# Kernel optimization log

Hardware: AMD Instinct MI355X
Metric: run time of the kernel (lower is better)

Reference implementation:

```python
import jax, jax.numpy as jnp
import numpy as np

N_NODES = 50000
E_HALF = 500000
N_FEAT = 5
GCN_DIMS = [32, 64, 128]
MLP_DIMS = [128, 64]


def _lin_init(key, fan_in, fan_out):
    return jax.random.normal(key, (fan_in, fan_out), dtype=jnp.float32) / np.sqrt(fan_in)


def setup_inputs() -> dict:
    key = jax.random.key(0)
    ks = jax.random.split(key, 20)
    x = jax.random.normal(ks[0], (N_NODES, N_FEAT), dtype=jnp.float32)
    src = jax.random.randint(ks[1], (E_HALF,), 0, N_NODES)
    dst = jax.random.randint(ks[2], (E_HALF,), 0, N_NODES)
    # paired edges: second half is the reversed direction of the first half
    edges = jnp.stack([jnp.concatenate([src, dst]), jnp.concatenate([dst, src])], axis=0).astype(jnp.int64)
    edge_attr = jax.random.uniform(ks[3], (2 * E_HALF, 2), dtype=jnp.float32)
    detector_labels = jnp.ones((N_NODES,), dtype=bool)
    inp = {"x": x, "edges": edges, "edge_attr": edge_attr, "detector_labels": detector_labels}
    # GraphConv params: out = agg @ w_rel + x @ w_root + b
    dims = [N_FEAT] + GCN_DIMS
    for i, (di, do) in enumerate(zip(dims[:-1], dims[1:])):
        inp[f"w_rel{i}"] = _lin_init(ks[4 + 3 * i], di, do)
        inp[f"w_root{i}"] = _lin_init(ks[5 + 3 * i], di, do)
        inp[f"b{i}"] = jnp.zeros((do,), dtype=jnp.float32)
    # edge MLP: transition_dim = 2*128 + 1 = 257
    mdims = [2 * GCN_DIMS[-1] + 1] + MLP_DIMS
    for i, (di, do) in enumerate(zip(mdims[:-1], mdims[1:])):
        inp[f"w_d{i}"] = _lin_init(ks[13 + 2 * i], di, do)
        inp[f"b_d{i}"] = jnp.zeros((do,), dtype=jnp.float32)
    inp["w_out"] = _lin_init(ks[17], MLP_DIMS[-1], 1)
    inp["b_out"] = jnp.zeros((1,), dtype=jnp.float32)
    return inp


def reference(x, edges, edge_attr, detector_labels,
              w_rel0, w_root0, b0, w_rel1, w_root1, b1, w_rel2, w_root2, b2,
              w_d0, b_d0, w_d1, b_d1, w_out, b_out):
    n = x.shape[0]
    src, dst = edges[0], edges[1]
    w = edge_attr[:, 0] * edge_attr[:, 1]  # [E]

    def gconv(h, wr, wro, b):
        msg = h[src] * w[:, None]                                   # gather + scale  [E, d]
        agg = jax.ops.segment_sum(msg, dst, num_segments=n)          # scatter-add     [N, d]
        return jnp.tanh(agg @ wr + h @ wro + b)

    h = gconv(x, w_rel0, w_root0, b0)
    h = gconv(h, w_rel1, w_root1, b1)
    h = gconv(h, w_rel2, w_root2, b2)

    # SplitSyndromes: keep edges whose both endpoints are detector nodes
    # (indices are concrete, so this is computed with numpy -> static shapes)
    e_np = np.asarray(edges)
    subset = np.arange(n)[np.asarray(detector_labels)]
    valid = np.isin(e_np, subset).sum(axis=0) == 2
    keep = np.nonzero(valid)[0]
    edges_f = jnp.asarray(e_np[:, keep])
    ea = edge_attr[keep]

    ef = jnp.concatenate([h[edges_f[0]], ea[:, :1], h[edges_f[1]]], axis=-1)  # [Ef, 257]
    ef = jnp.tanh(ef @ w_d0 + b_d0)
    ef = jnp.tanh(ef @ w_d1 + b_d1)
    ef = ef @ w_out + b_out                                                   # [Ef, 1]

    half = ef.shape[0] // 2
    ef2 = ef.reshape(2, half)
    classes = ea[:, 1].reshape(2, half)
    mi = jnp.argmin(ef2, axis=0)                                              # [half]
    ef_sel = jnp.take_along_axis(ef2, mi[None, :], axis=0)[0]
    cls_sel = jnp.take_along_axis(classes, mi[None, :], axis=0)[0]
    return edges_f[:, :half], ef_sel, cls_sel
```

## Files before the change

### kernel.cpp

```cpp
#include <hip/hip_runtime.h>
#include <hip/hip_bf16.h>


typedef __attribute__((ext_vector_type(8))) short short8;
typedef __attribute__((ext_vector_type(4))) float f32x4;

__device__ __forceinline__ float fast_tanh(float x) {
    float e = __expf(2.0f * x);
    return 1.0f - 2.0f * __builtin_amdgcn_rcpf(e + 1.0f);
}
__device__ __forceinline__ float b2f(unsigned short u) {
    union { unsigned i; float f; } c; c.i = ((unsigned)u) << 16; return c.f;
}
__device__ __forceinline__ short f2b(float f) {
    __hip_bfloat16 h = __float2bfloat16(f);
    return *reinterpret_cast<short*>(&h);
}
__device__ __forceinline__ float ldf(float v) { return v; }
__device__ __forceinline__ float ldf(unsigned short v) { return b2f(v); }


__global__ void deg_count(const int* __restrict__ ed, int* __restrict__ deg, int E) {
    int e = blockIdx.x * blockDim.x + threadIdx.x;
    if (e < E) atomicAdd(&deg[ed[E + e]], 1);
}

__global__ __launch_bounds__(1024) void scan_build(const int* __restrict__ deg,
                                                   int* __restrict__ off, int* __restrict__ cur,
                                                   int n) {
    __shared__ int part[1024];
    const int tid = threadIdx.x;
    const int chunk = (n + 1023) >> 10;
    const int b = tid * chunk;
    int s = 0;
    for (int i = 0; i < chunk; ++i) {
        int j = b + i;
        if (j < n) s += deg[j];
    }
    part[tid] = s;
    __syncthreads();
    for (int d = 1; d < 1024; d <<= 1) {
        int v = (tid >= d) ? part[tid - d] : 0;
        __syncthreads();
        part[tid] += v;
        __syncthreads();
    }
    int run = tid ? part[tid - 1] : 0;
    for (int i = 0; i < chunk; ++i) {
        int j = b + i;
        if (j < n) {
            off[j] = run;
            cur[j] = run;
            run += deg[j];
        }
    }
    if (tid == 1023) off[n] = run;
}

__global__ void csr_fill(const int* __restrict__ ed, const float* __restrict__ ea,
                         int* __restrict__ cur, int* __restrict__ srcl,
                         float* __restrict__ wl, int* __restrict__ eidl,
                         float* __restrict__ eal, int E) {
    int e = blockIdx.x * blockDim.x + threadIdx.x;
    if (e >= E) return;
    int d = ed[E + e];
    int pos = atomicAdd(&cur[d], 1);
    srcl[pos] = ed[e];
    wl[pos] = ea[2 * e] * ea[2 * e + 1];
    eidl[pos] = e;
    eal[pos] = ea[2 * e];
}


__global__ void gather_agg5(const float* __restrict__ x, const int* __restrict__ off,
                            const int* __restrict__ srcl, const float* __restrict__ wl,
                            float* __restrict__ agg, int n) {
    int node = blockIdx.x * blockDim.x + threadIdx.x;
    if (node >= n) return;
    int b = off[node], en = off[node + 1];
    float a0 = 0, a1 = 0, a2 = 0, a3 = 0, a4 = 0;
    for (int j = b; j < en; ++j) {
        int s = srcl[j];
        float w = wl[j];
        const float* xs = &x[(size_t)s * 5];
        a0 += xs[0] * w; a1 += xs[1] * w; a2 += xs[2] * w;
        a3 += xs[3] * w; a4 += xs[4] * w;
    }
    float* ag = &agg[(size_t)node * 5];
    ag[0] = a0; ag[1] = a1; ag[2] = a2; ag[3] = a3; ag[4] = a4;
}

template <int D>
__global__ void gather_agg_b(const unsigned short* __restrict__ h, const int* __restrict__ off,
                             const int* __restrict__ srcl, const float* __restrict__ wl,
                             float* __restrict__ agg, int n) {
    constexpr int TPN = D / 8;
    int idx = blockIdx.x * blockDim.x + threadIdx.x;
    int node = idx / TPN;
    int q = idx % TPN;
    if (node >= n) return;
    int b = off[node], en = off[node + 1];
    float acc[8] = {0, 0, 0, 0, 0, 0, 0, 0};
    for (int j = b; j < en; ++j) {
        int s = srcl[j];
        float w = wl[j];
        short8 v = *(const short8*)&h[(size_t)s * D + q * 8];
#pragma unroll
        for (int m = 0; m < 8; ++m) acc[m] += b2f((unsigned short)v[m]) * w;
    }
    float4* ag = (float4*)&agg[(size_t)node * D + q * 8];
    ag[0] = make_float4(acc[0], acc[1], acc[2], acc[3]);
    ag[1] = make_float4(acc[4], acc[5], acc[6], acc[7]);
}


template <int DIN, int DOUT, typename TI>
__global__ void node_update_b(const TI* __restrict__ hin, const float* __restrict__ agg,
                              const float* __restrict__ wrel, const float* __restrict__ wroot,
                              const float* __restrict__ bias, unsigned short* __restrict__ hout,
                              int n) {
    int idx = blockIdx.x * blockDim.x + threadIdx.x;
    if (idx >= n * DOUT) return;
    int node = idx / DOUT;
    int c = idx - node * DOUT;
    const float* ag = agg + (size_t)node * DIN;
    const TI* hi = hin + (size_t)node * DIN;
    float acc = bias[c];
#pragma unroll
    for (int k = 0; k < DIN; ++k)
        acc += ag[k] * wrel[k * DOUT + c] + ldf(hi[k]) * wroot[k * DOUT + c];
    hout[idx] = (unsigned short)f2b(fast_tanh(acc));
}


__global__ void prep_weights(const float* __restrict__ wd0, const float* __restrict__ wd1,
                             unsigned short* __restrict__ w0t, unsigned short* __restrict__ w1t) {
    int idx = blockIdx.x * blockDim.x + threadIdx.x;
    if (idx < 128 * 256) {
        int c = idx >> 8, k = idx & 255;
        int kr = (k < 128) ? k : k + 1;
        w0t[idx] = (unsigned short)f2b(wd0[(size_t)kr * 128 + c]);
    } else {
        int j = idx - 128 * 256;
        if (j < 64 * 128) {
            int c = j >> 7, k = j & 127;
            w1t[j] = (unsigned short)f2b(wd1[(size_t)k * 64 + c]);
        }
    }
}


__global__ __launch_bounds__(256) void uv_gemm(
    const unsigned short* __restrict__ h3b, const unsigned short* __restrict__ w0t,
    unsigned short* __restrict__ Ub, unsigned short* __restrict__ Vb, int n) {
    __shared__ __align__(16) unsigned short A[64 * 152];

    const int tid = threadIdx.x;
    const int wid = tid >> 6;
    const int lane = tid & 63;
    const int l15 = lane & 15;
    const int g = lane >> 4;
    const int base = blockIdx.x * 64;

#pragma unroll
    for (int i = 0; i < 4; ++i) {
        int cid = i * 256 + tid;
        int row = cid >> 4;
        int c8 = cid & 15;
        int node = base + row;
        if (node >= n) node = n - 1;
        *(short8*)&A[row * 152 + c8 * 8] = *(const short8*)&h3b[(size_t)node * 128 + c8 * 8];
    }

    const int koff = (wid < 2) ? 0 : 128;
    short8 bf[4][4];
#pragma unroll
    for (int ct = 0; ct < 4; ++ct) {
        int c = ((wid & 1) * 64 + 16 * ct + l15);
#pragma unroll
        for (int ks = 0; ks < 4; ++ks)
            bf[ct][ks] = *(const short8*)&w0t[(size_t)c * 256 + koff + ks * 32 + g * 8];
    }
    __syncthreads();

    f32x4 acc[4][4];
#pragma unroll
    for (int rt = 0; rt < 4; ++rt)
#pragma unroll
        for (int ct = 0; ct < 4; ++ct) acc[rt][ct] = (f32x4){0.f, 0.f, 0.f, 0.f};

#pragma unroll
    for (int rt = 0; rt < 4; ++rt) {
        short8 af[4];
#pragma unroll
        for (int ks = 0; ks < 4; ++ks)
            af[ks] = *(const short8*)&A[(16 * rt + l15) * 152 + ks * 32 + g * 8];
#pragma unroll
        for (int ct = 0; ct < 4; ++ct)
#pragma unroll
            for (int ks = 0; ks < 4; ++ks)
                acc[rt][ct] = __builtin_amdgcn_mfma_f32_16x16x32_bf16(af[ks], bf[ct][ks],
                                                                     acc[rt][ct], 0, 0, 0);
    }

    unsigned short* outp = (wid < 2) ? Ub : Vb;
    const int cb = (wid & 1) * 64;
#pragma unroll
    for (int rt = 0; rt < 4; ++rt)
#pragma unroll
        for (int ct = 0; ct < 4; ++ct) {
            int c = cb + 16 * ct + l15;
#pragma unroll
            for (int j = 0; j < 4; ++j) {
                int node = base + 16 * rt + 4 * g + j;
                if (node < n) outp[(size_t)node * 128 + c] = (unsigned short)f2b(acc[rt][ct][j]);
            }
        }
}


__global__ __launch_bounds__(256) void edge_mlp_uv(
    const unsigned short* __restrict__ Ub, const unsigned short* __restrict__ Vb,
    const int* __restrict__ srcl, const int* __restrict__ eidl, const int* __restrict__ off,
    int n, const float* __restrict__ eal, const unsigned short* __restrict__ w1t,
    const float* __restrict__ wd0, const float* __restrict__ bd0,
    const float* __restrict__ bd1, const float* __restrict__ wout,
    const float* __restrict__ bout, float* __restrict__ ef, int E) {
    __shared__ int SRC[64], DST[64], EID[64];
    __shared__ float EAs[64], WEA[128], B0F[128], B1[64], WOUT[64];

    const int tid = threadIdx.x;
    const int wid = tid >> 6;
    const int lane = tid & 63;
    const int l15 = lane & 15;
    const int g = lane >> 4;
    const int geb = blockIdx.x * 64;

    if (tid < 64) {
        int p = geb + tid;
        SRC[tid] = srcl[p];
        EID[tid] = eidl[p];
        EAs[tid] = eal[p];
        int lo = 0, hi = n;
        while (hi - lo > 1) {
            int mid = (lo + hi) >> 1;
            if (off[mid] <= p) lo = mid; else hi = mid;
        }
        DST[tid] = lo;
    } else if (tid < 192) {
        int c = tid - 64;
        WEA[c] = wd0[(size_t)128 * 128 + c];
        B0F[c] = bd0[c];
    } else {
        int c = tid - 192;
        B1[c] = bd1[c];
        WOUT[c] = wout[c];
    }
    __syncthreads();

    short8 bf[4][4];
#pragma unroll
    for (int ct = 0; ct < 4; ++ct)
#pragma unroll
        for (int ks = 0; ks < 4; ++ks)
            bf[ct][ks] = *(const short8*)&w1t[(size_t)(16 * ct + l15) * 128 + ks * 32 + g * 8];

    const int r = 16 * wid + l15;
    const int src = SRC[r], dst = DST[r];
    const float eav = EAs[r];

    f32x4 acc1[4];
#pragma unroll
    for (int ct = 0; ct < 4; ++ct) acc1[ct] = (f32x4){0.f, 0.f, 0.f, 0.f};

#pragma unroll
    for (int ks = 0; ks < 4; ++ks) {
        short8 u = *(const short8*)&Ub[(size_t)src * 128 + ks * 32 + g * 8];
        short8 v = *(const short8*)&Vb[(size_t)dst * 128 + ks * 32 + g * 8];
        short8 af;
#pragma unroll
        for (int m = 0; m < 8; ++m) {
            int kk = ks * 32 + g * 8 + m;
            float o = b2f((unsigned short)u[m]) + b2f((unsigned short)v[m]) +
                      eav * WEA[kk] + B0F[kk];
            af[m] = f2b(fast_tanh(o));
        }
#pragma unroll
        for (int ct = 0; ct < 4; ++ct)
            acc1[ct] = __builtin_amdgcn_mfma_f32_16x16x32_bf16(af, bf[ct][ks], acc1[ct], 0, 0, 0);
    }

    float p4[4] = {0.f, 0.f, 0.f, 0.f};
#pragma unroll
    for (int ct = 0; ct < 4; ++ct) {
        int col = 16 * ct + l15;
        float b1v = B1[col], wo = WOUT[col];
#pragma unroll
        for (int j = 0; j < 4; ++j) p4[j] += fast_tanh(acc1[ct][j] + b1v) * wo;
    }
#pragma unroll
    for (int j = 0; j < 4; ++j) {
        p4[j] += __shfl_xor(p4[j], 1);
        p4[j] += __shfl_xor(p4[j], 2);
        p4[j] += __shfl_xor(p4[j], 4);
        p4[j] += __shfl_xor(p4[j], 8);
    }
    if (l15 == 0) {
        float bo = bout[0];
#pragma unroll
        for (int j = 0; j < 4; ++j) ef[EID[16 * wid + 4 * g + j]] = p4[j] + bo;
    }
}


__global__ void finalize(const int* __restrict__ ed, const float* __restrict__ ea,
                         const float* __restrict__ ef, float* __restrict__ out,
                         int half, int E) {
    int i = blockIdx.x * blockDim.x + threadIdx.x;
    if (i >= half) return;
    float f0 = ef[i];
    float f1 = ef[i + half];
    int mi = (f1 < f0) ? 1 : 0;
    float fs = mi ? f1 : f0;
    float cs = ea[2 * (i + mi * half) + 1];
    out[i] = (float)ed[i];
    out[half + i] = (float)ed[E + i];
    out[2 * half + i] = fs;
    out[3 * half + i] = cs;
}


extern "C" void kernel_launch(void* const* d_in, const int* in_sizes, int n_in,
                              void* d_out, int out_size, void* d_ws, size_t ws_size,
                              hipStream_t stream) {
    const float* x = (const float*)d_in[0];
    const int* edges = (const int*)d_in[1];
    const float* ea = (const float*)d_in[2];
    const float* w_rel0 = (const float*)d_in[4];
    const float* w_root0 = (const float*)d_in[5];
    const float* b0 = (const float*)d_in[6];
    const float* w_rel1 = (const float*)d_in[7];
    const float* w_root1 = (const float*)d_in[8];
    const float* b1 = (const float*)d_in[9];
    const float* w_rel2 = (const float*)d_in[10];
    const float* w_root2 = (const float*)d_in[11];
    const float* b2 = (const float*)d_in[12];
    const float* w_d0 = (const float*)d_in[13];
    const float* b_d0 = (const float*)d_in[14];
    const float* w_d1 = (const float*)d_in[15];
    const float* b_d1 = (const float*)d_in[16];
    const float* w_out = (const float*)d_in[17];
    const float* b_out = (const float*)d_in[18];

    const int n = in_sizes[0] / 5;
    const int E = in_sizes[2] / 2;
    const int half = E / 2;

    float* ws = (float*)d_ws;
    size_t o_srcl = (size_t)n * 64;
    size_t o_eidl = o_srcl + E;
    size_t o_off  = o_eidl + E;
    size_t o_cur  = o_off + 51000;
    size_t o_deg  = o_cur + 50000;
    size_t o_eal  = o_deg + 50000;
    size_t o_w0t  = o_eal + E;
    size_t o_w1t  = o_w0t + 16384;

    unsigned short* h1b = (unsigned short*)ws;
    unsigned short* h3b = (unsigned short*)ws;
    float* ef = ws;
    int* srcl = (int*)(ws + o_srcl);
    int* eidl = (int*)(ws + o_eidl);
    int* off = (int*)(ws + o_off);
    int* cur = (int*)(ws + o_cur);
    int* deg = (int*)(ws + o_deg);
    float* eal = ws + o_eal;
    unsigned short* w0t = (unsigned short*)(ws + o_w0t);
    unsigned short* w1t = (unsigned short*)(ws + o_w1t);
    unsigned short* h2b = (unsigned short*)(ws + (size_t)n * 128);
    float* wl = ws + (size_t)n * 160;
    unsigned short* Ub = (unsigned short*)(ws + (size_t)n * 128);
    float* agg = ws + (size_t)n * 192;
    unsigned short* Vb = (unsigned short*)(ws + (size_t)n * 192);

    float* out = (float*)d_out;
    const int B = 256;

    hipMemsetAsync(deg, 0, (size_t)n * sizeof(int), stream);
    deg_count<<<(E + B - 1) / B, B, 0, stream>>>(edges, deg, E);
    scan_build<<<1, 1024, 0, stream>>>(deg, off, cur, n);
    csr_fill<<<(E + B - 1) / B, B, 0, stream>>>(edges, ea, cur, srcl, wl, eidl, eal, E);

    gather_agg5<<<(n + B - 1) / B, B, 0, stream>>>(x, off, srcl, wl, agg, n);
    node_update_b<5, 32, float><<<(n * 32 + B - 1) / B, B, 0, stream>>>(
        x, agg, w_rel0, w_root0, b0, h1b, n);

    gather_agg_b<32><<<((size_t)n * 4 + B - 1) / B, B, 0, stream>>>(h1b, off, srcl, wl, agg, n);
    node_update_b<32, 64, unsigned short><<<(n * 64 + B - 1) / B, B, 0, stream>>>(
        h1b, agg, w_rel1, w_root1, b1, h2b, n);

    gather_agg_b<64><<<((size_t)n * 8 + B - 1) / B, B, 0, stream>>>(h2b, off, srcl, wl, agg, n);
    node_update_b<64, 128, unsigned short><<<(n * 128 + B - 1) / B, B, 0, stream>>>(
        h2b, agg, w_rel2, w_root2, b2, h3b, n);

    prep_weights<<<160, B, 0, stream>>>(w_d0, w_d1, w0t, w1t);
    uv_gemm<<<(n + 63) / 64, B, 0, stream>>>(h3b, w0t, Ub, Vb, n);
    edge_mlp_uv<<<E / 64, B, 0, stream>>>(Ub, Vb, srcl, eidl, off, n, eal, w1t,
                                          w_d0, b_d0, b_d1, w_out, b_out, ef, E);

    finalize<<<(half + B - 1) / B, B, 0, stream>>>(edges, ea, ef, out, half, E);
}
```

Before: 813.2 us.

## Write edge MLP outputs in CSR order, fold bias into V, unroll gathers

The edge MLP now writes its output contiguously in CSR order rather than scattering through an edge-id list. csr_fill instead records each edge's CSR position, and finalize looks results up through it. The first-layer bias is folded into the V half of the UV GEMM, and the U/V loads in the edge MLP are hoisted ahead of the tanh loop. The gather kernels process two neighbours per iteration, and the 5-feature layer uses one thread per feature instead of one per node. The aim is fewer scattered writes, less shared-memory setup and more memory-level parallelism in the gathers. The cost is an indirect read in finalize.

```diff
diff --git a/kernel.cpp b/kernel.cpp
--- a/kernel.cpp
+++ b/kernel.cpp
@@ -59,7 +59,7 @@
 
 __global__ void csr_fill(const int* __restrict__ ed, const float* __restrict__ ea,
                          int* __restrict__ cur, int* __restrict__ srcl,
-                         float* __restrict__ wl, int* __restrict__ eidl,
+                         float* __restrict__ wl, int* __restrict__ posl,
                          float* __restrict__ eal, int E) {
     int e = blockIdx.x * blockDim.x + threadIdx.x;
     if (e >= E) return;
@@ -67,27 +67,28 @@
     int pos = atomicAdd(&cur[d], 1);
     srcl[pos] = ed[e];
     wl[pos] = ea[2 * e] * ea[2 * e + 1];
-    eidl[pos] = e;
     eal[pos] = ea[2 * e];
+    posl[e] = pos;
 }
 
 
 __global__ void gather_agg5(const float* __restrict__ x, const int* __restrict__ off,
                             const int* __restrict__ srcl, const float* __restrict__ wl,
                             float* __restrict__ agg, int n) {
-    int node = blockIdx.x * blockDim.x + threadIdx.x;
-    if (node >= n) return;
+    int idx = blockIdx.x * blockDim.x + threadIdx.x;
+    int node = idx >> 3;
+    int q = idx & 7;
+    if (node >= n || q >= 5) return;
     int b = off[node], en = off[node + 1];
-    float a0 = 0, a1 = 0, a2 = 0, a3 = 0, a4 = 0;
-    for (int j = b; j < en; ++j) {
-        int s = srcl[j];
-        float w = wl[j];
-        const float* xs = &x[(size_t)s * 5];
-        a0 += xs[0] * w; a1 += xs[1] * w; a2 += xs[2] * w;
-        a3 += xs[3] * w; a4 += xs[4] * w;
-    }
-    float* ag = &agg[(size_t)node * 5];
-    ag[0] = a0; ag[1] = a1; ag[2] = a2; ag[3] = a3; ag[4] = a4;
+    float acc = 0.f;
+    int j = b;
+    for (; j + 2 <= en; j += 2) {
+        int s0 = srcl[j], s1 = srcl[j + 1];
+        float w0 = wl[j], w1 = wl[j + 1];
+        acc += x[(size_t)s0 * 5 + q] * w0 + x[(size_t)s1 * 5 + q] * w1;
+    }
+    if (j < en) acc += x[(size_t)srcl[j] * 5 + q] * wl[j];
+    agg[(size_t)node * 5 + q] = acc;
 }
 
 template <int D>
@@ -101,7 +102,18 @@
     if (node >= n) return;
     int b = off[node], en = off[node + 1];
     float acc[8] = {0, 0, 0, 0, 0, 0, 0, 0};
-    for (int j = b; j < en; ++j) {
+    int j = b;
+#pragma unroll 1
+    for (; j + 2 <= en; j += 2) {
+        int s0 = srcl[j], s1 = srcl[j + 1];
+        float w0 = wl[j], w1 = wl[j + 1];
+        short8 v0 = *(const short8*)&h[(size_t)s0 * D + q * 8];
+        short8 v1 = *(const short8*)&h[(size_t)s1 * D + q * 8];
+#pragma unroll
+        for (int m = 0; m < 8; ++m)
+            acc[m] += b2f((unsigned short)v0[m]) * w0 + b2f((unsigned short)v1[m]) * w1;
+    }
+    if (j < en) {
         int s = srcl[j];
         float w = wl[j];
         short8 v = *(const short8*)&h[(size_t)s * D + q * 8];
@@ -152,6 +164,7 @@
 
 __global__ __launch_bounds__(256) void uv_gemm(
     const unsigned short* __restrict__ h3b, const unsigned short* __restrict__ w0t,
+    const float* __restrict__ bd0,
     unsigned short* __restrict__ Ub, unsigned short* __restrict__ Vb, int n) {
     __shared__ __align__(16) unsigned short A[64 * 152];
 
@@ -205,6 +218,10 @@
 
     unsigned short* outp = (wid < 2) ? Ub : Vb;
     const int cb = (wid & 1) * 64;
+    float b0v[4];
+#pragma unroll
+    for (int ct = 0; ct < 4; ++ct)
+        b0v[ct] = (wid < 2) ? 0.f : bd0[cb + 16 * ct + l15];
 #pragma unroll
     for (int rt = 0; rt < 4; ++rt)
 #pragma unroll
@@ -213,7 +230,8 @@
 #pragma unroll
             for (int j = 0; j < 4; ++j) {
                 int node = base + 16 * rt + 4 * g + j;
-                if (node < n) outp[(size_t)node * 128 + c] = (unsigned short)f2b(acc[rt][ct][j]);
+                if (node < n)
+                    outp[(size_t)node * 128 + c] = (unsigned short)f2b(acc[rt][ct][j] + b0v[ct]);
             }
         }
 }
@@ -221,13 +239,13 @@
 
 __global__ __launch_bounds__(256) void edge_mlp_uv(
     const unsigned short* __restrict__ Ub, const unsigned short* __restrict__ Vb,
-    const int* __restrict__ srcl, const int* __restrict__ eidl, const int* __restrict__ off,
+    const int* __restrict__ srcl, const int* __restrict__ off,
     int n, const float* __restrict__ eal, const unsigned short* __restrict__ w1t,
-    const float* __restrict__ wd0, const float* __restrict__ bd0,
+    const float* __restrict__ wd0,
     const float* __restrict__ bd1, const float* __restrict__ wout,
     const float* __restrict__ bout, float* __restrict__ ef, int E) {
-    __shared__ int SRC[64], DST[64], EID[64];
-    __shared__ float EAs[64], WEA[128], B0F[128], B1[64], WOUT[64];
+    __shared__ int SRC[64], DST[64];
+    __shared__ float EAs[64], WEA[128], B1[64], WOUT[64];
 
     const int tid = threadIdx.x;
     const int wid = tid >> 6;
@@ -239,7 +257,6 @@
     if (tid < 64) {
         int p = geb + tid;
         SRC[tid] = srcl[p];
-        EID[tid] = eidl[p];
         EAs[tid] = eal[p];
         int lo = 0, hi = n;
         while (hi - lo > 1) {
@@ -250,7 +267,6 @@
     } else if (tid < 192) {
         int c = tid - 64;
         WEA[c] = wd0[(size_t)128 * 128 + c];
-        B0F[c] = bd0[c];
     } else {
         int c = tid - 192;
         B1[c] = bd1[c];
@@ -269,20 +285,24 @@
     const int src = SRC[r], dst = DST[r];
     const float eav = EAs[r];
 
+    short8 u[4], v[4];
+#pragma unroll
+    for (int ks = 0; ks < 4; ++ks) {
+        u[ks] = *(const short8*)&Ub[(size_t)src * 128 + ks * 32 + g * 8];
+        v[ks] = *(const short8*)&Vb[(size_t)dst * 128 + ks * 32 + g * 8];
+    }
+
     f32x4 acc1[4];
 #pragma unroll
     for (int ct = 0; ct < 4; ++ct) acc1[ct] = (f32x4){0.f, 0.f, 0.f, 0.f};
 
 #pragma unroll
     for (int ks = 0; ks < 4; ++ks) {
-        short8 u = *(const short8*)&Ub[(size_t)src * 128 + ks * 32 + g * 8];
-        short8 v = *(const short8*)&Vb[(size_t)dst * 128 + ks * 32 + g * 8];
         short8 af;
 #pragma unroll
         for (int m = 0; m < 8; ++m) {
             int kk = ks * 32 + g * 8 + m;
-            float o = b2f((unsigned short)u[m]) + b2f((unsigned short)v[m]) +
-                      eav * WEA[kk] + B0F[kk];
+            float o = b2f((unsigned short)u[ks][m]) + b2f((unsigned short)v[ks][m]) + eav * WEA[kk];
             af[m] = f2b(fast_tanh(o));
         }
 #pragma unroll
@@ -308,18 +328,18 @@
     if (l15 == 0) {
         float bo = bout[0];
 #pragma unroll
-        for (int j = 0; j < 4; ++j) ef[EID[16 * wid + 4 * g + j]] = p4[j] + bo;
+        for (int j = 0; j < 4; ++j) ef[geb + 16 * wid + 4 * g + j] = p4[j] + bo;
     }
 }
 
 
 __global__ void finalize(const int* __restrict__ ed, const float* __restrict__ ea,
-                         const float* __restrict__ ef, float* __restrict__ out,
-                         int half, int E) {
+                         const float* __restrict__ ef, const int* __restrict__ posl,
+                         float* __restrict__ out, int half, int E) {
     int i = blockIdx.x * blockDim.x + threadIdx.x;
     if (i >= half) return;
-    float f0 = ef[i];
-    float f1 = ef[i + half];
+    float f0 = ef[posl[i]];
+    float f1 = ef[posl[i + half]];
     int mi = (f1 < f0) ? 1 : 0;
     float fs = mi ? f1 : f0;
     float cs = ea[2 * (i + mi * half) + 1];
@@ -358,8 +378,8 @@
 
     float* ws = (float*)d_ws;
     size_t o_srcl = (size_t)n * 64;
-    size_t o_eidl = o_srcl + E;
-    size_t o_off  = o_eidl + E;
+    size_t o_posl = o_srcl + E;
+    size_t o_off  = o_posl + E;
     size_t o_cur  = o_off + 51000;
     size_t o_deg  = o_cur + 50000;
     size_t o_eal  = o_deg + 50000;
@@ -370,7 +390,7 @@
     unsigned short* h3b = (unsigned short*)ws;
     float* ef = ws;
     int* srcl = (int*)(ws + o_srcl);
-    int* eidl = (int*)(ws + o_eidl);
+    int* posl = (int*)(ws + o_posl);
     int* off = (int*)(ws + o_off);
     int* cur = (int*)(ws + o_cur);
     int* deg = (int*)(ws + o_deg);
@@ -389,9 +409,9 @@
     hipMemsetAsync(deg, 0, (size_t)n * sizeof(int), stream);
     deg_count<<<(E + B - 1) / B, B, 0, stream>>>(edges, deg, E);
     scan_build<<<1, 1024, 0, stream>>>(deg, off, cur, n);
-    csr_fill<<<(E + B - 1) / B, B, 0, stream>>>(edges, ea, cur, srcl, wl, eidl, eal, E);
-
-    gather_agg5<<<(n + B - 1) / B, B, 0, stream>>>(x, off, srcl, wl, agg, n);
+    csr_fill<<<(E + B - 1) / B, B, 0, stream>>>(edges, ea, cur, srcl, wl, posl, eal, E);
+
+    gather_agg5<<<((size_t)n * 8 + B - 1) / B, B, 0, stream>>>(x, off, srcl, wl, agg, n);
     node_update_b<5, 32, float><<<(n * 32 + B - 1) / B, B, 0, stream>>>(
         x, agg, w_rel0, w_root0, b0, h1b, n);
 
@@ -404,9 +424,9 @@
         h2b, agg, w_rel2, w_root2, b2, h3b, n);
 
     prep_weights<<<160, B, 0, stream>>>(w_d0, w_d1, w0t, w1t);
-    uv_gemm<<<(n + 63) / 64, B, 0, stream>>>(h3b, w0t, Ub, Vb, n);
-    edge_mlp_uv<<<E / 64, B, 0, stream>>>(Ub, Vb, srcl, eidl, off, n, eal, w1t,
-                                          w_d0, b_d0, b_d1, w_out, b_out, ef, E);
-
-    finalize<<<(half + B - 1) / B, B, 0, stream>>>(edges, ea, ef, out, half, E);
-}
+    uv_gemm<<<(n + 63) / 64, B, 0, stream>>>(h3b, w0t, b_d0, Ub, Vb, n);
+    edge_mlp_uv<<<E / 64, B, 0, stream>>>(Ub, Vb, srcl, off, n, eal, w1t,
+                                          w_d0, b_d1, w_out, b_out, ef, E);
+
+    finalize<<<(half + B - 1) / B, B, 0, stream>>>(edges, ea, ef, posl, out, half, E);
+}
```

New measurement: 794.9 us. 1.02x faster.
